# Performance work log

Measured on AMD Instinct MI355X. Metric: run time of the kernel, lower is better.

Reference implementation:

```python
import jax, jax.numpy as jnp
import numpy as np

NUM_HEADS = 4
FEAT_DIM = 128
EMBED_DIM = 128
B, K, C, H, W = 2, 8, 128, 128, 128


def _cross_attn(Qf, Kf, Vf, qw, qb, kw, kb, aqw, aqb, akw, akb):
    """Faithful port of PixelCrossAttentionRefiner._cross_attn.
    Qf: [B, Cq, H, W]; Kf: [B, K, Ck, H, W]; Vf: [B, K, C, H, W].
    Uses only the (head-averaged) softmax weights of MultiheadAttention,
    L2-renormalizes them, then takes a weighted sum of RAW values.
    """
    b, _, h, w = Qf.shape
    k_cand = Kf.shape[1]
    bn = b * h * w
    # Query: per-pixel feature vector -> q1 projection -> attn in-proj (query part)
    Query = jnp.transpose(Qf, (0, 2, 3, 1)).reshape(bn, -1)            # [BN, Cq]
    q = Query @ qw.T + qb                                               # [BN, E]
    # Key: NOTE torch does .permute(0,1,3,4,2).reshape(B*N, K, -1) which is a
    # flat row-major reinterpretation of the (B,K,H,W,Ck) buffer; jnp reshape
    # after transpose has identical semantics, so this is bit-faithful.
    Key = jnp.transpose(Kf, (0, 1, 3, 4, 2)).reshape(bn, k_cand, -1)    # [BN, K, Ck]
    kk = Key @ kw.T + kb                                                # [BN, K, E]
    # nn.MultiheadAttention internal in-projections (value path is dead code)
    qa = q @ aqw.T + aqb                                                # [BN, E]
    ka = kk @ akw.T + akb                                               # [BN, K, E]
    e = qa.shape[-1]
    dh = e // NUM_HEADS
    qh = qa.reshape(bn, NUM_HEADS, dh)
    kh = ka.reshape(bn, k_cand, NUM_HEADS, dh)
    scale = 1.0 / np.sqrt(dh).astype(np.float32)
    scores = jnp.einsum('mhd,mkhd->mhk', qh, kh) * scale                # [BN, H, K]
    attw = jax.nn.softmax(scores, axis=-1).mean(axis=1)                 # avg heads -> [BN, K]
    # F.normalize(p=2, dim=-1, eps=1e-12)
    attw = attw / jnp.maximum(jnp.linalg.norm(attw, axis=-1, keepdims=True), 1e-12)
    Value = jnp.transpose(Vf, (0, 1, 3, 4, 2)).reshape(bn, k_cand, -1)  # [BN, K, C]
    out = jnp.einsum('mk,mkc->mc', attw, Value)                         # [BN, C]
    return jnp.transpose(out.reshape(b, h, w, -1), (0, 3, 1, 2))        # [B, C, H, W]


def _forward(HF_star, HF_cands, Z_cands,
             q1_w, q1_b, k1_w, k1_b, a1_qw, a1_qb, a1_kw, a1_kb,
             q2_w, q2_b, k2_w, k2_b, a2_qw, a2_qb, a2_kw, a2_kb):
    b, c, h, w = HF_star.shape
    k_cand = HF_cands.shape[1]
    i = jnp.linspace(0.0, 1.0, h, dtype=HF_star.dtype)
    j = jnp.linspace(0.0, 1.0, w, dtype=HF_star.dtype)
    ig, jg = jnp.meshgrid(i, j, indexing='ij')
    ig = jnp.broadcast_to(ig[None, None], (b, 1, h, w))
    jg = jnp.broadcast_to(jg[None, None], (b, 1, h, w))
    Q1 = jnp.concatenate([HF_star, ig, jg], axis=1)                     # [B, C+2, H, W]
    ik = jnp.broadcast_to(ig[:, None], (b, k_cand, 1, h, w))
    jk = jnp.broadcast_to(jg[:, None], (b, k_cand, 1, h, w))
    K1 = jnp.concatenate([HF_cands, ik, jk], axis=2)                    # [B, K, C+2, H, W]
    z_star = _cross_attn(Q1, K1, Z_cands, q1_w, q1_b, k1_w, k1_b,
                         a1_qw, a1_qb, a1_kw, a1_kb)                    # [B, C, H, W]
    z_exp = jnp.broadcast_to(z_star[:, None], (b, k_cand, c, h, w))
    Q2 = jnp.concatenate([HF_star, z_star, ig, jg], axis=1)             # [B, 2C+2, H, W]
    K2 = jnp.concatenate([HF_cands, z_exp, ik, jk], axis=2)             # [B, K, 2C+2, H, W]
    z_hat = _cross_attn(Q2, K2, Z_cands, q2_w, q2_b, k2_w, k2_b,
                        a2_qw, a2_qb, a2_kw, a2_kb)
    return z_star, z_hat


def setup_inputs() -> dict:
    key = jax.random.key(0)
    ks = jax.random.split(key, 16)
    E = EMBED_DIM
    d1 = FEAT_DIM + 2
    d2 = 2 * FEAT_DIM + 2

    def lin(k, fan_out, fan_in):
        bound = 1.0 / np.sqrt(fan_in)
        kw, kb = jax.random.split(k)
        return (jax.random.uniform(kw, (fan_out, fan_in), jnp.float32, -bound, bound),
                jax.random.uniform(kb, (fan_out,), jnp.float32, -bound, bound))

    q1_w, q1_b = lin(ks[0], E, d1)
    k1_w, k1_b = lin(ks[1], E, d1)
    q2_w, q2_b = lin(ks[2], E, d2)
    k2_w, k2_b = lin(ks[3], E, d2)
    a1_qw, a1_qb = lin(ks[4], E, E)
    a1_kw, a1_kb = lin(ks[5], E, E)
    a2_qw, a2_qb = lin(ks[6], E, E)
    a2_kw, a2_kb = lin(ks[7], E, E)
    return {
        'HF_star': jax.random.normal(ks[8], (B, C, H, W), jnp.float32),
        'HF_cands': jax.random.normal(ks[9], (B, K, C, H, W), jnp.float32),
        'Z_cands': jax.random.normal(ks[10], (B, K, C, H, W), jnp.float32),
        'q1_w': q1_w, 'q1_b': q1_b, 'k1_w': k1_w, 'k1_b': k1_b,
        'a1_qw': a1_qw, 'a1_qb': a1_qb, 'a1_kw': a1_kw, 'a1_kb': a1_kb,
        'q2_w': q2_w, 'q2_b': q2_b, 'k2_w': k2_w, 'k2_b': k2_b,
        'a2_qw': a2_qw, 'a2_qb': a2_qb, 'a2_kw': a2_kw, 'a2_kb': a2_kb,
    }


def reference(HF_star, HF_cands, Z_cands,
              q1_w, q1_b, k1_w, k1_b, a1_qw, a1_qb, a1_kw, a1_kb,
              q2_w, q2_b, k2_w, k2_b, a2_qw, a2_qb, a2_kw, a2_kb):
    return _forward(HF_star, HF_cands, Z_cands,
                    q1_w, q1_b, k1_w, k1_b, a1_qw, a1_qb, a1_kw, a1_kb,
                    q2_w, q2_b, k2_w, k2_b, a2_qw, a2_qb, a2_kw, a2_kb)
```

## Files before the change

### kernel.cpp

```cpp
#include <hip/hip_runtime.h>
#include <math.h>

constexpr int Bc = 2, Kc = 8, HWc = 16384;
constexpr float SCALE  = 0.17677669529663687f;
constexpr float INV127 = 1.0f / 127.0f;

using short8 = __attribute__((ext_vector_type(8))) short;
using f32x4  = __attribute__((ext_vector_type(4))) float;

constexpr int OWQ1 = 0;
constexpr int OBQ1 = OWQ1 + 130 * 128;
constexpr int OWK1 = OBQ1 + 128;
constexpr int OBK1 = OWK1 + 130 * 128;
constexpr int OWQ2 = OBK1 + 128;
constexpr int OBQ2 = OWQ2 + 258 * 128;
constexpr int OWK2 = OBQ2 + 128;
constexpr int OBK2 = OWK2 + 258 * 128;
constexpr int OPACK = OBK2 + 128;
constexpr int PQ1 = 0;
constexpr int PQ2 = PQ1 + 32 * 512;
constexpr int PY1 = PQ2 + 64 * 512;
constexpr int PY2 = PY1 + 32 * 512;

__device__ __forceinline__ unsigned bfpack(float a, float b) {
    unsigned ua = __float_as_uint(a); ua = (ua + 0x7FFFu + ((ua >> 16) & 1u)) >> 16;
    unsigned ub = __float_as_uint(b); ub = (ub + 0x7FFFu + ((ub >> 16) & 1u)) >> 16;
    return ua | (ub << 16);
}
__device__ __forceinline__ short bf1(float a) {
    unsigned ua = __float_as_uint(a); ua = (ua + 0x7FFFu + ((ua >> 16) & 1u)) >> 16;
    return (short)ua;
}
__device__ __forceinline__ float bflo(unsigned u) { return __uint_as_float(u << 16); }
__device__ __forceinline__ float bfhi(unsigned u) { return __uint_as_float(u & 0xFFFF0000u); }
__device__ __forceinline__ float bf2f(short s) {
    return __uint_as_float(((unsigned)(unsigned short)s) << 16);
}

__device__ __forceinline__ void fma16(float (&a)[4][4], uint2 u, float4 x) {
    const float y0 = bflo(u.x), y1 = bfhi(u.x), y2 = bflo(u.y), y3 = bfhi(u.y);
    a[0][0] += y0 * x.x; a[0][1] += y0 * x.y; a[0][2] += y0 * x.z; a[0][3] += y0 * x.w;
    a[1][0] += y1 * x.x; a[1][1] += y1 * x.y; a[1][2] += y1 * x.z; a[1][3] += y1 * x.w;
    a[2][0] += y2 * x.x; a[2][1] += y2 * x.y; a[2][2] += y2 * x.z; a[2][3] += y2 * x.w;
    a[3][0] += y3 * x.x; a[3][1] += y3 * x.y; a[3][2] += y3 * x.z; a[3][3] += y3 * x.w;
}

__global__ __launch_bounds__(128) void prep_kernel(
    const float* __restrict__ q1w, const float* __restrict__ q1b,
    const float* __restrict__ k1w, const float* __restrict__ k1b,
    const float* __restrict__ a1qw, const float* __restrict__ a1qb,
    const float* __restrict__ a1kw, const float* __restrict__ a1kb,
    const float* __restrict__ q2w, const float* __restrict__ q2b,
    const float* __restrict__ k2w, const float* __restrict__ k2b,
    const float* __restrict__ a2qw, const float* __restrict__ a2qb,
    const float* __restrict__ a2kw, const float* __restrict__ a2kb,
    float* __restrict__ ws)
{
    const int job = blockIdx.x / 260;
    const int d   = blockIdx.x % 260;
    const float *aw, *ab, *w, *wb;
    float *owt, *ob;
    int D;
    if (job == 0)      { aw=a1qw; ab=a1qb; w=q1w; wb=q1b; owt=ws+OWQ1; ob=ws+OBQ1; D=130; }
    else if (job == 1) { aw=a1kw; ab=a1kb; w=k1w; wb=k1b; owt=ws+OWK1; ob=ws+OBK1; D=130; }
    else if (job == 2) { aw=a2qw; ab=a2qb; w=q2w; wb=q2b; owt=ws+OWQ2; ob=ws+OBQ2; D=258; }
    else               { aw=a2kw; ab=a2kb; w=k2w; wb=k2b; owt=ws+OWK2; ob=ws+OBK2; D=258; }
    const int e = threadIdx.x;
    if (d < D) {
        float acc = 0.f;
        for (int f = 0; f < 128; ++f) acc += aw[e * 128 + f] * w[f * D + d];
        owt[d * 128 + e] = acc;
    } else if (d == D) {
        float acc = ab[e];
        for (int f = 0; f < 128; ++f) acc += aw[e * 128 + f] * wb[f];
        ob[e] = acc;
    }
}

__global__ __launch_bounds__(64) void pack_kernel(float* __restrict__ ws)
{
    short* pk = (short*)(ws + OPACK);
    const int l = threadIdx.x, bid = blockIdx.x;
    const float* w;
    short* dst;
    short v[8];
    if (bid < 32) {
        const int et = bid >> 2, kt = bid & 3;
        w = ws + OWQ1;
        dst = pk + PQ1 + ((size_t)(et * 4 + kt) * 64 + l) * 8;
        #pragma unroll
        for (int idx = 0; idx < 8; ++idx)
            v[idx] = bf1(w[(kt * 32 + (l >> 4) * 8 + idx) * 128 + et * 16 + (l & 15)]);
    } else if (bid < 96) {
        const int b2 = bid - 32, et = b2 >> 3, kt = b2 & 7;
        w = ws + OWQ2;
        dst = pk + PQ2 + ((size_t)(et * 8 + kt) * 64 + l) * 8;
        #pragma unroll
        for (int idx = 0; idx < 8; ++idx)
            v[idx] = bf1(w[(kt * 32 + (l >> 4) * 8 + idx) * 128 + et * 16 + (l & 15)]);
    } else if (bid < 128) {
        const int b2 = bid - 96, ct = b2 >> 2, h = b2 & 3;
        w = ws + OWK1;
        dst = pk + PY1 + ((size_t)(ct * 4 + h) * 64 + l) * 8;
        #pragma unroll
        for (int idx = 0; idx < 8; ++idx)
            v[idx] = bf1(w[(ct * 16 + (l & 15)) * 128 + h * 32 + (l >> 4) * 8 + idx]);
    } else {
        const int b2 = bid - 128, ct = b2 >> 2, h = b2 & 3;
        w = ws + OWK2;
        dst = pk + PY2 + ((size_t)(ct * 4 + h) * 64 + l) * 8;
        #pragma unroll
        for (int idx = 0; idx < 8; ++idx)
            v[idx] = bf1(w[(ct * 16 + (l & 15)) * 128 + h * 32 + (l >> 4) * 8 + idx]);
    }
    uint4 u;
    u.x = (unsigned)(unsigned short)v[0] | ((unsigned)(unsigned short)v[1] << 16);
    u.y = (unsigned)(unsigned short)v[2] | ((unsigned)(unsigned short)v[3] << 16);
    u.z = (unsigned)(unsigned short)v[4] | ((unsigned)(unsigned short)v[5] << 16);
    u.w = (unsigned)(unsigned short)v[6] | ((unsigned)(unsigned short)v[7] << 16);
    *(uint4*)dst = u;
}

template <int STAGE>
__global__ __launch_bounds__(256) void stage_kernel(
    const float* __restrict__ HFs,
    const float* __restrict__ HFc,
    const float* __restrict__ Zc,
    const float* __restrict__ ws,
    const float* __restrict__ zst,
    float* __restrict__ out)
{
    constexpr int CQ  = (STAGE == 1) ? 128 : 256;
    constexpr int CK  = CQ;
    constexpr int NP  = CK / 128;
    constexpr int NKT = CQ / 32;
    constexpr int UNION_B = CK * 16 * 8;

    const float* qwt = ws + ((STAGE == 1) ? OWQ1 : OWQ2);
    const float* qb_ = ws + ((STAGE == 1) ? OBQ1 : OBQ2);
    const float* kwt = ws + ((STAGE == 1) ? OWK1 : OWK2);
    const float* kb_ = ws + ((STAGE == 1) ? OBK1 : OBK2);
    const short* pk  = (const short*)(ws + OPACK);
    const short* aQ  = pk + ((STAGE == 1) ? PQ1 : PQ2);
    const short* aY  = pk + ((STAGE == 1) ? PY1 : PY2);

    __shared__ __align__(16) char smem[UNION_B + 768 + 2304 + 2048 + 512];
    short* sXF = (short*)smem;
    short* sQF = (short*)(smem + CQ * 32);
    uint2* sYQ = (uint2*)smem;
    float* sRed = (float*)smem;
    float* sYX = (float*)(smem + UNION_B);
    float* sHW = sYX + 192;
    float* sSc = sHW + 576;
    float* sAW = sSc + 512;

    const int t   = threadIdx.x;
    const int l   = t & 63;
    const int wv  = t >> 6;
    const int bid = blockIdx.x;
    const int b   = bid >> 10;
    const int rem = bid & 1023;
    const int ks  = rem >> 7;
    const int hp  = rem & 127;
    const int r0  = ks * 2048 + hp * 16;

    const float ik = (float)hp * INV127;
    const float iq = (float)(r0 >> 7) * INV127;
    const int   w0 = r0 & 127;

    {
        const int qg = t & 3, c = t >> 2;
        #pragma unroll
        for (int r = 0; r < CQ / 64; ++r) {
            const int cc = c + r * 64;
            const float* src = (STAGE == 1 || cc < 128)
                ? HFs + ((size_t)(b * 128 + cc)) * HWc + r0 + qg * 4
                : zst + ((size_t)(b * 128 + cc - 128)) * HWc + r0 + qg * 4;
            const float4 x = *(const float4*)src;
            const int kt = cc >> 5, g = (cc & 31) >> 3, idx = cc & 7;
            short* dstb = &sXF[kt * 512 + idx + 16 * g * 8];
            dstb[(qg * 4 + 0) * 8] = bf1(x.x);
            dstb[(qg * 4 + 1) * 8] = bf1(x.y);
            dstb[(qg * 4 + 2) * 8] = bf1(x.z);
            dstb[(qg * 4 + 3) * 8] = bf1(x.w);
        }
    }
    __syncthreads();

    {
        const float jqv = (float)(w0 + (l & 15)) * INV127;
        f32x4 acc0, acc1;
        #pragma unroll
        for (int r = 0; r < 4; ++r) {
            const int e0 = (wv * 2 + 0) * 16 + (l >> 4) * 4 + r;
            const int e1 = (wv * 2 + 1) * 16 + (l >> 4) * 4 + r;
            acc0[r] = qb_[e0] + iq * qwt[(size_t)CQ * 128 + e0]
                             + jqv * qwt[(size_t)(CQ + 1) * 128 + e0];
            acc1[r] = qb_[e1] + iq * qwt[(size_t)CQ * 128 + e1]
                             + jqv * qwt[(size_t)(CQ + 1) * 128 + e1];
        }
        #pragma unroll
        for (int kt = 0; kt < NKT; ++kt) {
            const short8 bfr = *(const short8*)&sXF[kt * 512 + l * 8];
            const short8 a0 = *(const short8*)&aQ[(((wv * 2 + 0) * NKT + kt) * 64 + l) * 8];
            const short8 a1 = *(const short8*)&aQ[(((wv * 2 + 1) * NKT + kt) * 64 + l) * 8];
            acc0 = __builtin_amdgcn_mfma_f32_16x16x32_bf16(a0, bfr, acc0, 0, 0, 0);
            acc1 = __builtin_amdgcn_mfma_f32_16x16x32_bf16(a1, bfr, acc1, 0, 0, 0);
        }
        __syncthreads();
        #pragma unroll
        for (int m = 0; m < 2; ++m) {
            const f32x4 a = m ? acc1 : acc0;
            const int e0 = (wv * 2 + m) * 16 + (l >> 4) * 4;
            const int kt = e0 >> 5, g = (e0 & 31) >> 3, idx0 = e0 & 7;
            uint2 u; u.x = bfpack(a[0], a[1]); u.y = bfpack(a[2], a[3]);
            *(uint2*)&sQF[kt * 512 + ((l & 15) + 16 * g) * 8 + idx0] = u;
        }
    }
    __syncthreads();

    if (t < 192) {
        const int qq = t & 15, h = (t >> 4) & 3, which = t >> 6;
        const float* wrow = (which == 0) ? kwt + (size_t)CK * 128
                          : (which == 1) ? kwt + (size_t)(CK + 1) * 128
                                         : kb_;
        float acc = 0.f;
        #pragma unroll
        for (int e32 = 0; e32 < 32; ++e32) {
            const int e2 = h * 32 + e32;
            const int g = (e2 & 31) >> 3, idx = e2 & 7;
            acc += wrow[e2] * bf2f(sQF[h * 512 + (qq + 16 * g) * 8 + idx]);
        }
        sYX[(which * 4 + h) * 16 + qq] = acc;
    }

    const short8 bq0 = *(const short8*)&sQF[0 * 512 + l * 8];
    const short8 bq1 = *(const short8*)&sQF[1 * 512 + l * 8];
    const short8 bq2 = *(const short8*)&sQF[2 * 512 + l * 8];
    const short8 bq3 = *(const short8*)&sQF[3 * 512 + l * 8];
    __syncthreads();

    {
        const f32x4 zf = {0.f, 0.f, 0.f, 0.f};
        #pragma unroll
        for (int p = 0; p < NP; ++p) {
            #pragma unroll
            for (int m = 0; m < 2; ++m) {
                const int ct = p * 8 + wv * 2 + m;
                const short8 y0 = *(const short8*)&aY[(((ct * 4) + 0) * 64 + l) * 8];
                const short8 y1 = *(const short8*)&aY[(((ct * 4) + 1) * 64 + l) * 8];
                const short8 y2 = *(const short8*)&aY[(((ct * 4) + 2) * 64 + l) * 8];
                const short8 y3 = *(const short8*)&aY[(((ct * 4) + 3) * 64 + l) * 8];
                f32x4 d0 = __builtin_amdgcn_mfma_f32_16x16x32_bf16(y0, bq0, zf, 0, 0, 0);
                f32x4 d1 = __builtin_amdgcn_mfma_f32_16x16x32_bf16(y1, bq1, zf, 0, 0, 0);
                f32x4 d2 = __builtin_amdgcn_mfma_f32_16x16x32_bf16(y2, bq2, zf, 0, 0, 0);
                f32x4 d3 = __builtin_amdgcn_mfma_f32_16x16x32_bf16(y3, bq3, zf, 0, 0, 0);
                #pragma unroll
                for (int r = 0; r < 4; ++r) {
                    const int cg = ct * 16 + (l >> 4) * 4 + r;
                    uint2 u;
                    u.x = bfpack(d0[r], d1[r]);
                    u.y = bfpack(d2[r], d3[r]);
                    sYQ[cg * 16 + (l & 15)] = u;
                }
            }
        }
    }
    __syncthreads();

    const int pg = t & 31;
    const int cs = t >> 5;
    const int q  = pg >> 1;
    float acc[4][4];
    #pragma unroll
    for (int h = 0; h < 4; ++h)
        #pragma unroll
        for (int j = 0; j < 4; ++j) acc[h][j] = 0.f;

    #pragma unroll
    for (int half = 0; half < NP; ++half) {
        const int cbase = half * 128 + cs * 16;
        const float* xp = (STAGE == 1 || half == 0)
            ? HFc + (((size_t)(b * Kc + ks)) * 128 + cbase) * HWc + hp * 128 + pg * 4
            : zst + ((size_t)(b * 128 + cs * 16)) * HWc + hp * 128 + pg * 4;
        const uint2* yqp = &sYQ[cbase * 16 + q];
        #pragma unroll 8
        for (int cc = 0; cc < 16; ++cc) {
            const float4 x = *(const float4*)(xp + (size_t)cc * HWc);
            fma16(acc, yqp[cc * 16], x);
        }
    }

    #pragma unroll
    for (int h = 0; h < 4; ++h)
        #pragma unroll
        for (int j = 0; j < 4; ++j)
            acc[h][j] += __shfl_xor(acc[h][j], 32, 64);
    __syncthreads();
    if (l < 32) {
        #pragma unroll
        for (int h = 0; h < 4; ++h)
            #pragma unroll
            for (int j = 0; j < 4; ++j)
                sRed[wv * 512 + pg * 16 + h * 4 + j] = acc[h][j];
    }
    __syncthreads();

    if (t < 128) {
        const int pos = t, pgg = pos >> 2, j = pos & 3, qq = pos >> 3;
        const float jk = (float)pos * INV127;
        #pragma unroll
        for (int h = 0; h < 4; ++h) {
            const float v = sRed[0 * 512 + pgg * 16 + h * 4 + j]
                          + sRed[1 * 512 + pgg * 16 + h * 4 + j]
                          + sRed[2 * 512 + pgg * 16 + h * 4 + j]
                          + sRed[3 * 512 + pgg * 16 + h * 4 + j];
            const float s = v + ik * sYX[(0 * 4 + h) * 16 + qq]
                              + jk * sYX[(1 * 4 + h) * 16 + qq]
                              +      sYX[(2 * 4 + h) * 16 + qq];
            sSc[h * 128 + pos] = s * SCALE;
        }
    }
    __syncthreads();

    if (t < 64) {
        const int qq = t & 15, h = t >> 4;
        float sc[8], m = -INFINITY;
        #pragma unroll
        for (int j = 0; j < 8; ++j) {
            sc[j] = sSc[h * 128 + qq * 8 + j];
            m = fmaxf(m, sc[j]);
        }
        float sum = 0.f;
        #pragma unroll
        for (int j = 0; j < 8; ++j) { sc[j] = __expf(sc[j] - m); sum += sc[j]; }
        const float inv = 0.25f / sum;
        #pragma unroll
        for (int j = 0; j < 8; ++j) sHW[(h * 16 + qq) * 9 + j] = sc[j] * inv;
    }
    __syncthreads();
    if (t < 16) {
        float at[8];
        float n2 = 0.f;
        #pragma unroll
        for (int j = 0; j < 8; ++j) {
            at[j] = sHW[(0 * 16 + t) * 9 + j] + sHW[(1 * 16 + t) * 9 + j]
                  + sHW[(2 * 16 + t) * 9 + j] + sHW[(3 * 16 + t) * 9 + j];
            n2 += at[j] * at[j];
        }
        const float nrm = fmaxf(sqrtf(n2), 1e-12f);
        #pragma unroll
        for (int j = 0; j < 8; ++j) sAW[t * 8 + j] = at[j] / nrm;
    }
    __syncthreads();

    {
        const int idx = t & 15, cg = t >> 4;
        const int c8  = cg * 8;
        const float4 a0 = *(const float4*)&sAW[idx * 8];
        const float4 a1 = *(const float4*)&sAW[idx * 8 + 4];
        const float* zb = Zc + (((size_t)(b * Kc + ks)) * 128 + c8) * HWc + hp * 128 + idx * 8;
        float* ob = out + ((size_t)(b * 128 + c8)) * HWc + r0 + idx;
        #pragma unroll
        for (int i = 0; i < 8; ++i) {
            const float4 z0 = *(const float4*)(zb + (size_t)i * HWc);
            const float4 z1 = *(const float4*)(zb + (size_t)i * HWc + 4);
            ob[(size_t)i * HWc] =
                a0.x * z0.x + a0.y * z0.y + a0.z * z0.z + a0.w * z0.w +
                a1.x * z1.x + a1.y * z1.y + a1.z * z1.z + a1.w * z1.w;
        }
    }
}

extern "C" void kernel_launch(void* const* d_in, const int* in_sizes, int n_in,
                              void* d_out, int out_size, void* d_ws, size_t ws_size,
                              hipStream_t stream)
{
    const float* HFs = (const float*)d_in[0];
    const float* HFc = (const float*)d_in[1];
    const float* Zc  = (const float*)d_in[2];
    float* ws    = (float*)d_ws;
    float* zstar = (float*)d_out;
    float* zhat  = zstar + (size_t)Bc * 128 * HWc;

    prep_kernel<<<1040, 128, 0, stream>>>(
        (const float*)d_in[3],  (const float*)d_in[4],
        (const float*)d_in[5],  (const float*)d_in[6],
        (const float*)d_in[7],  (const float*)d_in[8],
        (const float*)d_in[9],  (const float*)d_in[10],
        (const float*)d_in[11], (const float*)d_in[12],
        (const float*)d_in[13], (const float*)d_in[14],
        (const float*)d_in[15], (const float*)d_in[16],
        (const float*)d_in[17], (const float*)d_in[18],
        ws);

    pack_kernel<<<192, 64, 0, stream>>>(ws);

    stage_kernel<1><<<2048, 256, 0, stream>>>(HFs, HFc, Zc, ws, zstar, zstar);
    stage_kernel<2><<<2048, 256, 0, stream>>>(HFs, HFc, Zc, ws, zstar, zhat);
}
```

Baseline: 150.8 us.

## Split stage-2 into projection, score, combine and PV kernels

Stage 1 becomes its own non-templated kernel, and stage 2 is split into four kernels: query projection, partial scores over channel halves (twice as many blocks), a combine/softmax kernel, and the weighted value sum. The aim is more parallelism and occupancy for the heavy stage-2 score reduction, which used to loop over both channel halves inside one block. In exchange, intermediates (projected queries, partial scores, attention weights) round-trip through global workspace and there are extra kernel launches.

```diff
diff --git a/kernel.cpp b/kernel.cpp
--- a/kernel.cpp
+++ b/kernel.cpp
@@ -21,6 +21,10 @@
 constexpr int PQ2 = PQ1 + 32 * 512;
 constexpr int PY1 = PQ2 + 64 * 512;
 constexpr int PY2 = PY1 + 32 * 512;
+constexpr int OQA2  = OPACK + 49152;
+constexpr int OYX2  = OQA2 + 2048 * 2048 / 2;
+constexpr int OPART = OYX2 + 2048 * 192;
+constexpr int OATTW = OPART + 4096 * 512;
 
 __device__ __forceinline__ unsigned bfpack(float a, float b) {
     unsigned ua = __float_as_uint(a); ua = (ua + 0x7FFFu + ((ua >> 16) & 1u)) >> 16;
@@ -121,28 +125,25 @@
     *(uint4*)dst = u;
 }
 
-template <int STAGE>
-__global__ __launch_bounds__(256) void stage_kernel(
+__global__ __launch_bounds__(256) void stage1_kernel(
     const float* __restrict__ HFs,
     const float* __restrict__ HFc,
     const float* __restrict__ Zc,
     const float* __restrict__ ws,
-    const float* __restrict__ zst,
     float* __restrict__ out)
 {
-    constexpr int CQ  = (STAGE == 1) ? 128 : 256;
-    constexpr int CK  = CQ;
-    constexpr int NP  = CK / 128;
-    constexpr int NKT = CQ / 32;
+    constexpr int CQ  = 128;
+    constexpr int CK  = 128;
+    constexpr int NKT = 4;
     constexpr int UNION_B = CK * 16 * 8;
 
-    const float* qwt = ws + ((STAGE == 1) ? OWQ1 : OWQ2);
-    const float* qb_ = ws + ((STAGE == 1) ? OBQ1 : OBQ2);
-    const float* kwt = ws + ((STAGE == 1) ? OWK1 : OWK2);
-    const float* kb_ = ws + ((STAGE == 1) ? OBK1 : OBK2);
+    const float* qwt = ws + OWQ1;
+    const float* qb_ = ws + OBQ1;
+    const float* kwt = ws + OWK1;
+    const float* kb_ = ws + OBK1;
     const short* pk  = (const short*)(ws + OPACK);
-    const short* aQ  = pk + ((STAGE == 1) ? PQ1 : PQ2);
-    const short* aY  = pk + ((STAGE == 1) ? PY1 : PY2);
+    const short* aQ  = pk + PQ1;
+    const short* aY  = pk + PY1;
 
     __shared__ __align__(16) char smem[UNION_B + 768 + 2304 + 2048 + 512];
     short* sXF = (short*)smem;
@@ -173,7 +174,236 @@
         #pragma unroll
         for (int r = 0; r < CQ / 64; ++r) {
             const int cc = c + r * 64;
-            const float* src = (STAGE == 1 || cc < 128)
+            const float* src = HFs + ((size_t)(b * 128 + cc)) * HWc + r0 + qg * 4;
+            const float4 x = *(const float4*)src;
+            const int kt = cc >> 5, g = (cc & 31) >> 3, idx = cc & 7;
+            short* dstb = &sXF[kt * 512 + idx + 16 * g * 8];
+            dstb[(qg * 4 + 0) * 8] = bf1(x.x);
+            dstb[(qg * 4 + 1) * 8] = bf1(x.y);
+            dstb[(qg * 4 + 2) * 8] = bf1(x.z);
+            dstb[(qg * 4 + 3) * 8] = bf1(x.w);
+        }
+    }
+    __syncthreads();
+
+    {
+        const float jqv = (float)(w0 + (l & 15)) * INV127;
+        f32x4 acc0, acc1;
+        #pragma unroll
+        for (int r = 0; r < 4; ++r) {
+            const int e0 = (wv * 2 + 0) * 16 + (l >> 4) * 4 + r;
+            const int e1 = (wv * 2 + 1) * 16 + (l >> 4) * 4 + r;
+            acc0[r] = qb_[e0] + iq * qwt[(size_t)CQ * 128 + e0]
+                             + jqv * qwt[(size_t)(CQ + 1) * 128 + e0];
+            acc1[r] = qb_[e1] + iq * qwt[(size_t)CQ * 128 + e1]
+                             + jqv * qwt[(size_t)(CQ + 1) * 128 + e1];
+        }
+        #pragma unroll
+        for (int kt = 0; kt < NKT; ++kt) {
+            const short8 bfr = *(const short8*)&sXF[kt * 512 + l * 8];
+            const short8 a0 = *(const short8*)&aQ[(((wv * 2 + 0) * NKT + kt) * 64 + l) * 8];
+            const short8 a1 = *(const short8*)&aQ[(((wv * 2 + 1) * NKT + kt) * 64 + l) * 8];
+            acc0 = __builtin_amdgcn_mfma_f32_16x16x32_bf16(a0, bfr, acc0, 0, 0, 0);
+            acc1 = __builtin_amdgcn_mfma_f32_16x16x32_bf16(a1, bfr, acc1, 0, 0, 0);
+        }
+        __syncthreads();
+        #pragma unroll
+        for (int m = 0; m < 2; ++m) {
+            const f32x4 a = m ? acc1 : acc0;
+            const int e0 = (wv * 2 + m) * 16 + (l >> 4) * 4;
+            const int kt = e0 >> 5, g = (e0 & 31) >> 3, idx0 = e0 & 7;
+            uint2 u; u.x = bfpack(a[0], a[1]); u.y = bfpack(a[2], a[3]);
+            *(uint2*)&sQF[kt * 512 + ((l & 15) + 16 * g) * 8 + idx0] = u;
+        }
+    }
+    __syncthreads();
+
+    if (t < 192) {
+        const int qq = t & 15, h = (t >> 4) & 3, which = t >> 6;
+        const float* wrow = (which == 0) ? kwt + (size_t)CK * 128
+                          : (which == 1) ? kwt + (size_t)(CK + 1) * 128
+                                         : kb_;
+        float acc = 0.f;
+        #pragma unroll
+        for (int e32 = 0; e32 < 32; ++e32) {
+            const int e2 = h * 32 + e32;
+            const int g = (e2 & 31) >> 3, idx = e2 & 7;
+            acc += wrow[e2] * bf2f(sQF[h * 512 + (qq + 16 * g) * 8 + idx]);
+        }
+        sYX[(which * 4 + h) * 16 + qq] = acc;
+    }
+
+    const short8 bq0 = *(const short8*)&sQF[0 * 512 + l * 8];
+    const short8 bq1 = *(const short8*)&sQF[1 * 512 + l * 8];
+    const short8 bq2 = *(const short8*)&sQF[2 * 512 + l * 8];
+    const short8 bq3 = *(const short8*)&sQF[3 * 512 + l * 8];
+    __syncthreads();
+
+    {
+        const f32x4 zf = {0.f, 0.f, 0.f, 0.f};
+        #pragma unroll
+        for (int m = 0; m < 2; ++m) {
+            const int ct = wv * 2 + m;
+            const short8 y0 = *(const short8*)&aY[(((ct * 4) + 0) * 64 + l) * 8];
+            const short8 y1 = *(const short8*)&aY[(((ct * 4) + 1) * 64 + l) * 8];
+            const short8 y2 = *(const short8*)&aY[(((ct * 4) + 2) * 64 + l) * 8];
+            const short8 y3 = *(const short8*)&aY[(((ct * 4) + 3) * 64 + l) * 8];
+            f32x4 d0 = __builtin_amdgcn_mfma_f32_16x16x32_bf16(y0, bq0, zf, 0, 0, 0);
+            f32x4 d1 = __builtin_amdgcn_mfma_f32_16x16x32_bf16(y1, bq1, zf, 0, 0, 0);
+            f32x4 d2 = __builtin_amdgcn_mfma_f32_16x16x32_bf16(y2, bq2, zf, 0, 0, 0);
+            f32x4 d3 = __builtin_amdgcn_mfma_f32_16x16x32_bf16(y3, bq3, zf, 0, 0, 0);
+            #pragma unroll
+            for (int r = 0; r < 4; ++r) {
+                const int cg = ct * 16 + (l >> 4) * 4 + r;
+                uint2 u;
+                u.x = bfpack(d0[r], d1[r]);
+                u.y = bfpack(d2[r], d3[r]);
+                sYQ[cg * 16 + (l & 15)] = u;
+            }
+        }
+    }
+    __syncthreads();
+
+    const int pg = t & 31;
+    const int cs = t >> 5;
+    const int q  = pg >> 1;
+    float acc[4][4];
+    #pragma unroll
+    for (int h = 0; h < 4; ++h)
+        #pragma unroll
+        for (int j = 0; j < 4; ++j) acc[h][j] = 0.f;
+    {
+        const int cbase = cs * 16;
+        const float* xp = HFc + (((size_t)(b * Kc + ks)) * 128 + cbase) * HWc
+                        + hp * 128 + pg * 4;
+        const uint2* yqp = &sYQ[cbase * 16 + q];
+        #pragma unroll 8
+        for (int cc = 0; cc < 16; ++cc) {
+            const float4 x = *(const float4*)(xp + (size_t)cc * HWc);
+            fma16(acc, yqp[cc * 16], x);
+        }
+    }
+
+    #pragma unroll
+    for (int h = 0; h < 4; ++h)
+        #pragma unroll
+        for (int j = 0; j < 4; ++j)
+            acc[h][j] += __shfl_xor(acc[h][j], 32, 64);
+    __syncthreads();
+    if (l < 32) {
+        #pragma unroll
+        for (int h = 0; h < 4; ++h)
+            #pragma unroll
+            for (int j = 0; j < 4; ++j)
+                sRed[wv * 512 + pg * 16 + h * 4 + j] = acc[h][j];
+    }
+    __syncthreads();
+
+    if (t < 128) {
+        const int pos = t, pgg = pos >> 2, j = pos & 3, qq = pos >> 3;
+        const float jk = (float)pos * INV127;
+        #pragma unroll
+        for (int h = 0; h < 4; ++h) {
+            const float v = sRed[0 * 512 + pgg * 16 + h * 4 + j]
+                          + sRed[1 * 512 + pgg * 16 + h * 4 + j]
+                          + sRed[2 * 512 + pgg * 16 + h * 4 + j]
+                          + sRed[3 * 512 + pgg * 16 + h * 4 + j];
+            const float s = v + ik * sYX[(0 * 4 + h) * 16 + qq]
+                              + jk * sYX[(1 * 4 + h) * 16 + qq]
+                              +      sYX[(2 * 4 + h) * 16 + qq];
+            sSc[h * 128 + pos] = s * SCALE;
+        }
+    }
+    __syncthreads();
+
+    if (t < 64) {
+        const int qq = t & 15, h = t >> 4;
+        float sc[8], m = -INFINITY;
+        #pragma unroll
+        for (int j = 0; j < 8; ++j) {
+            sc[j] = sSc[h * 128 + qq * 8 + j];
+            m = fmaxf(m, sc[j]);
+        }
+        float sum = 0.f;
+        #pragma unroll
+        for (int j = 0; j < 8; ++j) { sc[j] = __expf(sc[j] - m); sum += sc[j]; }
+        const float inv = 0.25f / sum;
+        #pragma unroll
+        for (int j = 0; j < 8; ++j) sHW[(h * 16 + qq) * 9 + j] = sc[j] * inv;
+    }
+    __syncthreads();
+    if (t < 16) {
+        float at[8];
+        float n2 = 0.f;
+        #pragma unroll
+        for (int j = 0; j < 8; ++j) {
+            at[j] = sHW[(0 * 16 + t) * 9 + j] + sHW[(1 * 16 + t) * 9 + j]
+                  + sHW[(2 * 16 + t) * 9 + j] + sHW[(3 * 16 + t) * 9 + j];
+            n2 += at[j] * at[j];
+        }
+        const float nrm = fmaxf(sqrtf(n2), 1e-12f);
+        #pragma unroll
+        for (int j = 0; j < 8; ++j) sAW[t * 8 + j] = at[j] / nrm;
+    }
+    __syncthreads();
+
+    {
+        const int idx = t & 15, cg = t >> 4;
+        const int c8  = cg * 8;
+        const float4 a0 = *(const float4*)&sAW[idx * 8];
+        const float4 a1 = *(const float4*)&sAW[idx * 8 + 4];
+        const float* zb = Zc + (((size_t)(b * Kc + ks)) * 128 + c8) * HWc + hp * 128 + idx * 8;
+        float* ob = out + ((size_t)(b * 128 + c8)) * HWc + r0 + idx;
+        #pragma unroll
+        for (int i = 0; i < 8; ++i) {
+            const float4 z0 = *(const float4*)(zb + (size_t)i * HWc);
+            const float4 z1 = *(const float4*)(zb + (size_t)i * HWc + 4);
+            ob[(size_t)i * HWc] =
+                a0.x * z0.x + a0.y * z0.y + a0.z * z0.z + a0.w * z0.w +
+                a1.x * z1.x + a1.y * z1.y + a1.z * z1.z + a1.w * z1.w;
+        }
+    }
+}
+
+__global__ __launch_bounds__(256) void s2_proj_kernel(
+    const float* __restrict__ HFs,
+    const float* __restrict__ ws_c,
+    const float* __restrict__ zst,
+    float* __restrict__ ws)
+{
+    constexpr int CQ  = 256;
+    constexpr int CK  = 256;
+    constexpr int NKT = 8;
+
+    const float* qwt = ws_c + OWQ2;
+    const float* qb_ = ws_c + OBQ2;
+    const float* kwt = ws_c + OWK2;
+    const float* kb_ = ws_c + OBK2;
+    const short* aQ  = (const short*)(ws_c + OPACK) + PQ2;
+
+    __shared__ __align__(16) char smem[CQ * 32 + 4096 + 768];
+    short* sXF = (short*)smem;
+    short* sQF = (short*)(smem + CQ * 32);
+    float* sYX = (float*)(smem + CQ * 32 + 4096);
+
+    const int t   = threadIdx.x;
+    const int l   = t & 63;
+    const int wv  = t >> 6;
+    const int bid = blockIdx.x;
+    const int b   = bid >> 10;
+    const int rem = bid & 1023;
+    const int ks  = rem >> 7;
+    const int hp  = rem & 127;
+    const int r0  = ks * 2048 + hp * 16;
+    const float iq = (float)(r0 >> 7) * INV127;
+    const int   w0 = r0 & 127;
+
+    {
+        const int qg = t & 3, c = t >> 2;
+        #pragma unroll
+        for (int r = 0; r < 4; ++r) {
+            const int cc = c + r * 64;
+            const float* src = (cc < 128)
                 ? HFs + ((size_t)(b * 128 + cc)) * HWc + r0 + qg * 4
                 : zst + ((size_t)(b * 128 + cc - 128)) * HWc + r0 + qg * 4;
             const float4 x = *(const float4*)src;
@@ -207,7 +437,6 @@
             acc0 = __builtin_amdgcn_mfma_f32_16x16x32_bf16(a0, bfr, acc0, 0, 0, 0);
             acc1 = __builtin_amdgcn_mfma_f32_16x16x32_bf16(a1, bfr, acc1, 0, 0, 0);
         }
-        __syncthreads();
         #pragma unroll
         for (int m = 0; m < 2; ++m) {
             const f32x4 a = m ? acc1 : acc0;
@@ -233,36 +462,66 @@
         }
         sYX[(which * 4 + h) * 16 + qq] = acc;
     }
-
-    const short8 bq0 = *(const short8*)&sQF[0 * 512 + l * 8];
-    const short8 bq1 = *(const short8*)&sQF[1 * 512 + l * 8];
-    const short8 bq2 = *(const short8*)&sQF[2 * 512 + l * 8];
-    const short8 bq3 = *(const short8*)&sQF[3 * 512 + l * 8];
-    __syncthreads();
+    __syncthreads();
+
+    {
+        short* qaG = (short*)(ws + OQA2) + (size_t)bid * 2048;
+        *(uint4*)&qaG[t * 8] = *(const uint4*)&sQF[t * 8];
+        if (t < 192) ws[OYX2 + (size_t)bid * 192 + t] = sYX[t];
+    }
+}
+
+__global__ __launch_bounds__(256) void s2_score_kernel(
+    const float* __restrict__ HFc,
+    const float* __restrict__ ws_c,
+    const float* __restrict__ zst,
+    float* __restrict__ ws)
+{
+    const short* aY = (const short*)(ws_c + OPACK) + PY2;
+
+    __shared__ __align__(16) char smem[16384];
+    uint2* sYQ  = (uint2*)smem;
+    float* sRed = (float*)smem;
+
+    const int t   = threadIdx.x;
+    const int l   = t & 63;
+    const int wv  = t >> 6;
+    const int bid = blockIdx.x;
+    const int b     = bid >> 11;
+    const int rem   = bid & 2047;
+    const int ks    = rem >> 8;
+    const int rem2  = rem & 255;
+    const int hp    = rem2 >> 1;
+    const int chalf = rem2 & 1;
+    const int blk   = ((b * Kc + ks) << 7) + hp;
+
+    const short* qaG = (const short*)(ws_c + OQA2) + (size_t)blk * 2048;
+    const short8 bq0 = *(const short8*)&qaG[0 * 512 + l * 8];
+    const short8 bq1 = *(const short8*)&qaG[1 * 512 + l * 8];
+    const short8 bq2 = *(const short8*)&qaG[2 * 512 + l * 8];
+    const short8 bq3 = *(const short8*)&qaG[3 * 512 + l * 8];
 
     {
         const f32x4 zf = {0.f, 0.f, 0.f, 0.f};
         #pragma unroll
-        for (int p = 0; p < NP; ++p) {
+        for (int m = 0; m < 2; ++m) {
+            const int ctl = wv * 2 + m;
+            const int ct  = chalf * 8 + ctl;
+            const short8 y0 = *(const short8*)&aY[(((ct * 4) + 0) * 64 + l) * 8];
+            const short8 y1 = *(const short8*)&aY[(((ct * 4) + 1) * 64 + l) * 8];
+            const short8 y2 = *(const short8*)&aY[(((ct * 4) + 2) * 64 + l) * 8];
+            const short8 y3 = *(const short8*)&aY[(((ct * 4) + 3) * 64 + l) * 8];
+            f32x4 d0 = __builtin_amdgcn_mfma_f32_16x16x32_bf16(y0, bq0, zf, 0, 0, 0);
+            f32x4 d1 = __builtin_amdgcn_mfma_f32_16x16x32_bf16(y1, bq1, zf, 0, 0, 0);
+            f32x4 d2 = __builtin_amdgcn_mfma_f32_16x16x32_bf16(y2, bq2, zf, 0, 0, 0);
+            f32x4 d3 = __builtin_amdgcn_mfma_f32_16x16x32_bf16(y3, bq3, zf, 0, 0, 0);
             #pragma unroll
-            for (int m = 0; m < 2; ++m) {
-                const int ct = p * 8 + wv * 2 + m;
-                const short8 y0 = *(const short8*)&aY[(((ct * 4) + 0) * 64 + l) * 8];
-                const short8 y1 = *(const short8*)&aY[(((ct * 4) + 1) * 64 + l) * 8];
-                const short8 y2 = *(const short8*)&aY[(((ct * 4) + 2) * 64 + l) * 8];
-                const short8 y3 = *(const short8*)&aY[(((ct * 4) + 3) * 64 + l) * 8];
-                f32x4 d0 = __builtin_amdgcn_mfma_f32_16x16x32_bf16(y0, bq0, zf, 0, 0, 0);
-                f32x4 d1 = __builtin_amdgcn_mfma_f32_16x16x32_bf16(y1, bq1, zf, 0, 0, 0);
-                f32x4 d2 = __builtin_amdgcn_mfma_f32_16x16x32_bf16(y2, bq2, zf, 0, 0, 0);
-                f32x4 d3 = __builtin_amdgcn_mfma_f32_16x16x32_bf16(y3, bq3, zf, 0, 0, 0);
-                #pragma unroll
-                for (int r = 0; r < 4; ++r) {
-                    const int cg = ct * 16 + (l >> 4) * 4 + r;
-                    uint2 u;
-                    u.x = bfpack(d0[r], d1[r]);
-                    u.y = bfpack(d2[r], d3[r]);
-                    sYQ[cg * 16 + (l & 15)] = u;
-                }
+            for (int r = 0; r < 4; ++r) {
+                const int cl = ctl * 16 + (l >> 4) * 4 + r;
+                uint2 u;
+                u.x = bfpack(d0[r], d1[r]);
+                u.y = bfpack(d2[r], d3[r]);
+                sYQ[cl * 16 + (l & 15)] = u;
             }
         }
     }
@@ -276,14 +535,12 @@
     for (int h = 0; h < 4; ++h)
         #pragma unroll
         for (int j = 0; j < 4; ++j) acc[h][j] = 0.f;
-
-    #pragma unroll
-    for (int half = 0; half < NP; ++half) {
-        const int cbase = half * 128 + cs * 16;
-        const float* xp = (STAGE == 1 || half == 0)
-            ? HFc + (((size_t)(b * Kc + ks)) * 128 + cbase) * HWc + hp * 128 + pg * 4
-            : zst + ((size_t)(b * 128 + cs * 16)) * HWc + hp * 128 + pg * 4;
-        const uint2* yqp = &sYQ[cbase * 16 + q];
+    {
+        const int clocal = cs * 16;
+        const float* xp = (chalf == 0)
+            ? HFc + (((size_t)(b * Kc + ks)) * 128 + clocal) * HWc + hp * 128 + pg * 4
+            : zst + ((size_t)(b * 128 + clocal)) * HWc + hp * 128 + pg * 4;
+        const uint2* yqp = &sYQ[clocal * 16 + q];
         #pragma unroll 8
         for (int cc = 0; cc < 16; ++cc) {
             const float4 x = *(const float4*)(xp + (size_t)cc * HWc);
@@ -307,17 +564,44 @@
     __syncthreads();
 
     if (t < 128) {
-        const int pos = t, pgg = pos >> 2, j = pos & 3, qq = pos >> 3;
+        const int pos = t, pgg = pos >> 2, j = pos & 3;
+        float* pout = ws + OPART + ((size_t)blk * 2 + chalf) * 512;
+        #pragma unroll
+        for (int h = 0; h < 4; ++h) {
+            pout[h * 128 + pos] = sRed[0 * 512 + pgg * 16 + h * 4 + j]
+                                + sRed[1 * 512 + pgg * 16 + h * 4 + j]
+                                + sRed[2 * 512 + pgg * 16 + h * 4 + j]
+                                + sRed[3 * 512 + pgg * 16 + h * 4 + j];
+        }
+    }
+}
+
+__global__ __launch_bounds__(256) void s2_combine_kernel(
+    const float* __restrict__ ws_c, float* __restrict__ ws)
+{
+    __shared__ float sYX[192];
+    __shared__ float sSc[512];
+    __shared__ float sHW[576];
+
+    const int t   = threadIdx.x;
+    const int blk = blockIdx.x;
+    const int hp  = blk & 127;
+    const float ik = (float)hp * INV127;
+
+    if (t < 192) sYX[t] = ws_c[OYX2 + (size_t)blk * 192 + t];
+    __syncthreads();
+
+    if (t < 128) {
+        const int pos = t, qq = pos >> 3;
         const float jk = (float)pos * INV127;
+        const float* p0 = ws_c + OPART + ((size_t)blk * 2 + 0) * 512;
+        const float* p1 = ws_c + OPART + ((size_t)blk * 2 + 1) * 512;
         #pragma unroll
         for (int h = 0; h < 4; ++h) {
-            const float v = sRed[0 * 512 + pgg * 16 + h * 4 + j]
-                          + sRed[1 * 512 + pgg * 16 + h * 4 + j]
-                          + sRed[2 * 512 + pgg * 16 + h * 4 + j]
-                          + sRed[3 * 512 + pgg * 16 + h * 4 + j];
-            const float s = v + ik * sYX[(0 * 4 + h) * 16 + qq]
-                              + jk * sYX[(1 * 4 + h) * 16 + qq]
-                              +      sYX[(2 * 4 + h) * 16 + qq];
+            const float s = p0[h * 128 + pos] + p1[h * 128 + pos]
+                          + ik * sYX[(0 * 4 + h) * 16 + qq]
+                          + jk * sYX[(1 * 4 + h) * 16 + qq]
+                          +      sYX[(2 * 4 + h) * 16 + qq];
             sSc[h * 128 + pos] = s * SCALE;
         }
     }
@@ -350,25 +634,42 @@
         }
         const float nrm = fmaxf(sqrtf(n2), 1e-12f);
         #pragma unroll
-        for (int j = 0; j < 8; ++j) sAW[t * 8 + j] = at[j] / nrm;
-    }
-    __syncthreads();
-
-    {
-        const int idx = t & 15, cg = t >> 4;
-        const int c8  = cg * 8;
-        const float4 a0 = *(const float4*)&sAW[idx * 8];
-        const float4 a1 = *(const float4*)&sAW[idx * 8 + 4];
-        const float* zb = Zc + (((size_t)(b * Kc + ks)) * 128 + c8) * HWc + hp * 128 + idx * 8;
-        float* ob = out + ((size_t)(b * 128 + c8)) * HWc + r0 + idx;
-        #pragma unroll
-        for (int i = 0; i < 8; ++i) {
-            const float4 z0 = *(const float4*)(zb + (size_t)i * HWc);
-            const float4 z1 = *(const float4*)(zb + (size_t)i * HWc + 4);
-            ob[(size_t)i * HWc] =
-                a0.x * z0.x + a0.y * z0.y + a0.z * z0.z + a0.w * z0.w +
-                a1.x * z1.x + a1.y * z1.y + a1.z * z1.z + a1.w * z1.w;
-        }
+        for (int j = 0; j < 8; ++j)
+            ws[OATTW + (size_t)blk * 128 + t * 8 + j] = at[j] / nrm;
+    }
+}
+
+__global__ __launch_bounds__(256) void s2_pv_kernel(
+    const float* __restrict__ Zc,
+    const float* __restrict__ ws_c,
+    float* __restrict__ out)
+{
+    __shared__ __align__(16) float sAW[128];
+
+    const int t   = threadIdx.x;
+    const int blk = blockIdx.x;
+    const int b   = blk >> 10;
+    const int rem = blk & 1023;
+    const int ks  = rem >> 7;
+    const int hp  = rem & 127;
+    const int r0  = ks * 2048 + hp * 16;
+
+    if (t < 128) sAW[t] = ws_c[OATTW + (size_t)blk * 128 + t];
+    __syncthreads();
+
+    const int idx = t & 15, cg = t >> 4;
+    const int c8  = cg * 8;
+    const float4 a0 = *(const float4*)&sAW[idx * 8];
+    const float4 a1 = *(const float4*)&sAW[idx * 8 + 4];
+    const float* zb = Zc + (((size_t)(b * Kc + ks)) * 128 + c8) * HWc + hp * 128 + idx * 8;
+    float* ob = out + ((size_t)(b * 128 + c8)) * HWc + r0 + idx;
+    #pragma unroll
+    for (int i = 0; i < 8; ++i) {
+        const float4 z0 = *(const float4*)(zb + (size_t)i * HWc);
+        const float4 z1 = *(const float4*)(zb + (size_t)i * HWc + 4);
+        ob[(size_t)i * HWc] =
+            a0.x * z0.x + a0.y * z0.y + a0.z * z0.z + a0.w * z0.w +
+            a1.x * z1.x + a1.y * z1.y + a1.z * z1.z + a1.w * z1.w;
     }
 }
 
@@ -396,6 +697,10 @@
 
     pack_kernel<<<192, 64, 0, stream>>>(ws);
 
-    stage_kernel<1><<<2048, 256, 0, stream>>>(HFs, HFc, Zc, ws, zstar, zstar);
-    stage_kernel<2><<<2048, 256, 0, stream>>>(HFs, HFc, Zc, ws, zstar, zhat);
-}
+    stage1_kernel<<<2048, 256, 0, stream>>>(HFs, HFc, Zc, ws, zstar);
+
+    s2_proj_kernel<<<2048, 256, 0, stream>>>(HFs, ws, zstar, ws);
+    s2_score_kernel<<<4096, 256, 0, stream>>>(HFc, ws, zstar, ws);
+    s2_combine_kernel<<<2048, 256, 0, stream>>>(ws, ws);
+    s2_pv_kernel<<<2048, 256, 0, stream>>>(Zc, ws, zhat);
+}
```

New measurement: 171.8 us. +13.9%, slower.
